# Performance work log

Measured on AMD Instinct MI355X. Metric: run time of the kernel, lower is better.

## Reference

```python
import jax, jax.numpy as jnp
import numpy as np

NCODEBOOKS, K, SUBVEC = 32, 16, 128
IN_F, OUT_F = 4096, 2048
BATCH, SEQ = 2, 1024


def setup_inputs() -> dict:
    key = jax.random.key(0)
    k1, k2, k3, k4, k5 = jax.random.split(key, 5)
    return {
        "x": jax.random.normal(k1, (BATCH, SEQ, IN_F), dtype=jnp.float32),
        "centroids": jax.random.normal(k2, (NCODEBOOKS, K, SUBVEC), dtype=jnp.float32),
        "weight": jax.random.normal(k3, (NCODEBOOKS, SUBVEC, OUT_F), dtype=jnp.float32),
        "inverse_temperature_logit": jax.random.normal(k4, (1,), dtype=jnp.float32),
        "bias": jax.random.normal(k5, (OUT_F,), dtype=jnp.float32),
    }


def reference(x, centroids, weight, inverse_temperature_logit, bias):
    shape = x.shape[:-1]
    C, k, d = centroids.shape
    # [N, C, d] -> [C, N, d]
    xr = jnp.transpose(x.reshape(-1, C, d), (1, 0, 2))
    # Euclidean cdist per codebook: [C, N, k]
    x2 = jnp.sum(xr * xr, axis=-1)[:, :, None]
    c2 = jnp.sum(centroids * centroids, axis=-1)[:, None, :]
    xc = jnp.einsum('cnd,ckd->cnk', xr, centroids)
    dist = jnp.sqrt(jnp.maximum(x2 + c2 - 2.0 * xc, 0.0))
    inv_temp = jax.nn.softplus(inverse_temperature_logit) + 1.0  # [1]
    attention = jax.nn.softmax(-dist * inv_temp, axis=-1)  # [C, N, k]
    lut = jnp.einsum('ckd,cdo->cko', centroids, weight)  # [C, k, O]
    training_output = jnp.einsum('cnk,cko->no', attention, lut)  # [N, O]
    # one-hot argmin matmul == direct gather of lut rows
    idx = jnp.argmin(dist, axis=-1)  # [C, N]
    gathered = jnp.take_along_axis(lut, idx[:, :, None], axis=1)  # [C, N, O]
    inference_output = jnp.sum(gathered, axis=0)  # [N, O]
    # straight-through estimator
    output = training_output - jax.lax.stop_gradient(training_output - inference_output)
    output = output + bias
    return output.reshape(*shape, lut.shape[-1])
```

## Files before the change

kernel.cpp:

```cpp
#include <hip/hip_runtime.h>

#define NCB 32
#define KK 16
#define DD 128
#define IN_F 4096
#define OUT_F 2048
#define NTOK 2048

#define LUT_BLOCKS 128
#define TT 32
#define IDX_BLOCKS ((NTOK / TT) * NCB)

#define XS_STRIDE 148
#define CS_OFF (TT * XS_STRIDE)
#define SMEM_FLOATS (CS_OFF + KK * 164)

__global__ __launch_bounds__(256, 4) void fused_lut_idx(
    const float* __restrict__ centroids, const float* __restrict__ weight,
    const float* __restrict__ x, const float* __restrict__ bias,
    float* __restrict__ lut, unsigned char* __restrict__ idxb) {
    __shared__ float smem[SMEM_FLOATS];
    const int tid = threadIdx.x;

    if (blockIdx.x < LUT_BLOCKS) {
        const int c  = blockIdx.x >> 2;
        const int kh = (blockIdx.x >> 1) & 1;
        const int oh = blockIdx.x & 1;
        const int o  = oh * 1024 + tid * 4;
        const float* cb = centroids + ((size_t)c * KK + kh * 8) * DD;
        const float* wb = weight + (size_t)c * DD * OUT_F + o;
        float4 acc[8];
#pragma unroll
        for (int k = 0; k < 8; ++k) acc[k] = make_float4(0.f, 0.f, 0.f, 0.f);
#pragma unroll 2
        for (int d4 = 0; d4 < DD / 4; ++d4) {
            float4 w0 = *(const float4*)(wb + (size_t)(d4 * 4 + 0) * OUT_F);
            float4 w1 = *(const float4*)(wb + (size_t)(d4 * 4 + 1) * OUT_F);
            float4 w2 = *(const float4*)(wb + (size_t)(d4 * 4 + 2) * OUT_F);
            float4 w3 = *(const float4*)(wb + (size_t)(d4 * 4 + 3) * OUT_F);
#pragma unroll
            for (int k = 0; k < 8; ++k) {
                float4 cv = *(const float4*)(cb + k * DD + d4 * 4);
                acc[k].x += cv.x * w0.x + cv.y * w1.x + cv.z * w2.x + cv.w * w3.x;
                acc[k].y += cv.x * w0.y + cv.y * w1.y + cv.z * w2.y + cv.w * w3.y;
                acc[k].z += cv.x * w0.z + cv.y * w1.z + cv.z * w2.z + cv.w * w3.z;
                acc[k].w += cv.x * w0.w + cv.y * w1.w + cv.z * w2.w + cv.w * w3.w;
            }
        }
        if (c == 0) {
            float4 bv = *(const float4*)(bias + o);
#pragma unroll
            for (int k = 0; k < 8; ++k) {
                acc[k].x += bv.x; acc[k].y += bv.y;
                acc[k].z += bv.z; acc[k].w += bv.w;
            }
        }
#pragma unroll
        for (int k = 0; k < 8; ++k)
            *(float4*)(lut + ((size_t)c * KK + kh * 8 + k) * OUT_F + o) = acc[k];
    } else {
        const int bid = blockIdx.x - LUT_BLOCKS;
        const int c = bid & (NCB - 1);
        const int t0 = (bid >> 5) * TT;
        const int th_q = tid & 3;
        const int th_k = (tid >> 2) & 3;
        const int th_t = tid >> 4;
        float* xs = smem;
        float* cs = smem + CS_OFF;

        {
            const float* xg = x + (size_t)t0 * IN_F + c * DD;
#pragma unroll
            for (int i = 0; i < (TT * DD / 4) / 256; ++i) {
                int p = i * 256 + tid;
                int t = p >> 5, f4 = p & 31;
                int q = f4 >> 3, jj = f4 & 7;
                float4 v = *(const float4*)(xg + (size_t)t * IN_F + f4 * 4);
                *(float4*)(xs + t * XS_STRIDE + q * 36 + jj * 4) = v;
            }
        }
        for (int p = tid; p < KK * 32; p += 256) {
            int k = p >> 5, f4 = p & 31;
            int q = f4 >> 3, jj = f4 & 7;
            *(float4*)(cs + k * 164 + q * 40 + jj * 4) =
                *(const float4*)(centroids + ((size_t)c * KK + k) * DD + f4 * 4);
        }
        __syncthreads();

        float acc[2][4], sq[4];
#pragma unroll
        for (int r = 0; r < 2; ++r)
#pragma unroll
            for (int kk = 0; kk < 4; ++kk) acc[r][kk] = 0.f;
#pragma unroll
        for (int kk = 0; kk < 4; ++kk) sq[kk] = 0.f;

#pragma unroll
        for (int chunk = 0; chunk < 8; ++chunk) {
            float4 ca[4];
#pragma unroll
            for (int kk = 0; kk < 4; ++kk)
                ca[kk] = *(const float4*)(cs + (th_k * 4 + kk) * 164 + th_q * 40 + chunk * 4);
#pragma unroll
            for (int kk = 0; kk < 4; ++kk)
                sq[kk] += ca[kk].x * ca[kk].x + ca[kk].y * ca[kk].y
                        + ca[kk].z * ca[kk].z + ca[kk].w * ca[kk].w;
#pragma unroll
            for (int r = 0; r < 2; ++r) {
                float4 xr = *(const float4*)(xs + (th_t * 2 + r) * XS_STRIDE
                                             + th_q * 36 + chunk * 4);
#pragma unroll
                for (int kk = 0; kk < 4; ++kk)
                    acc[r][kk] += xr.x * ca[kk].x + xr.y * ca[kk].y
                                + xr.z * ca[kk].z + xr.w * ca[kk].w;
            }
        }
#pragma unroll
        for (int kk = 0; kk < 4; ++kk) {
            float a = sq[kk];
            a += __shfl_xor(a, 1);
            a += __shfl_xor(a, 2);
            sq[kk] = a;
        }
#pragma unroll
        for (int r = 0; r < 2; ++r)
#pragma unroll
            for (int kk = 0; kk < 4; ++kk) {
                float a = acc[r][kk];
                a += __shfl_xor(a, 1);
                a += __shfl_xor(a, 2);
                acc[r][kk] = a;
            }
#pragma unroll
        for (int r = 0; r < 2; ++r) {
            float best = sq[0] - 2.f * acc[r][0];
            int bi = th_k * 4;
#pragma unroll
            for (int kk = 1; kk < 4; ++kk) {
                float v = sq[kk] - 2.f * acc[r][kk];
                if (v < best) { best = v; bi = th_k * 4 + kk; }
            }
#pragma unroll
            for (int s = 4; s <= 8; s <<= 1) {
                float ov = __shfl_xor(best, s);
                int oi = __shfl_xor(bi, s);
                if (ov < best || (ov == best && oi < bi)) { best = ov; bi = oi; }
            }
            if ((tid & 15) == 0)
                idxb[(size_t)(t0 + th_t * 2 + r) * NCB + c] = (unsigned char)bi;
        }
    }
}

__global__ __launch_bounds__(256) void gather_kernel(const float* __restrict__ lut,
                                                     const unsigned char* __restrict__ idxb,
                                                     float* __restrict__ out) {
    const int o0 = blockIdx.x * 32;
    const int t0 = blockIdx.y * 128;
    const int og = threadIdx.x & 7;
    const int tl = threadIdx.x >> 3;
    const int o = o0 + og * 4;

#pragma unroll
    for (int tt = 0; tt < 4; ++tt) {
        const int t = t0 + tt * 32 + tl;
        const uint4 iv0 = *(const uint4*)(idxb + (size_t)t * NCB);
        const uint4 iv1 = *(const uint4*)(idxb + (size_t)t * NCB + 16);
        unsigned int u[8] = {iv0.x, iv0.y, iv0.z, iv0.w, iv1.x, iv1.y, iv1.z, iv1.w};
        float4 acc = make_float4(0.f, 0.f, 0.f, 0.f);
#pragma unroll
        for (int c4 = 0; c4 < 8; ++c4) {
            unsigned int uv = u[c4];
#pragma unroll
            for (int b = 0; b < 4; ++b) {
                int cc = c4 * 4 + b;
                int k = (uv >> (8 * b)) & 0xff;
                const float4 v = *(const float4*)(lut + (size_t)(cc * KK + k) * OUT_F + o);
                acc.x += v.x; acc.y += v.y; acc.z += v.z; acc.w += v.w;
            }
        }
        *(float4*)(out + (size_t)t * OUT_F + o) = acc;
    }
}

extern "C" void kernel_launch(void* const* d_in, const int* in_sizes, int n_in,
                              void* d_out, int out_size, void* d_ws, size_t ws_size,
                              hipStream_t stream) {
    const float* x         = (const float*)d_in[0];
    const float* centroids = (const float*)d_in[1];
    const float* weight    = (const float*)d_in[2];
    const float* bias      = (const float*)d_in[4];
    float* out = (float*)d_out;

    float* lut = (float*)d_ws;
    unsigned char* idxb = (unsigned char*)d_ws + (4u << 20);

    fused_lut_idx<<<LUT_BLOCKS + IDX_BLOCKS, 256, 0, stream>>>(
        centroids, weight, x, bias, lut, idxb);
    gather_kernel<<<dim3(OUT_F / 32, NTOK / 128), 256, 0, stream>>>(lut, idxb, out);
}
```

Measured before the change: 141.0 us.

## Load x and centroids directly from global in idx path; interleave gather over two tokens

```diff
diff --git a/kernel.cpp b/kernel.cpp
--- a/kernel.cpp
+++ b/kernel.cpp
@@ -11,15 +11,10 @@
 #define TT 32
 #define IDX_BLOCKS ((NTOK / TT) * NCB)
 
-#define XS_STRIDE 148
-#define CS_OFF (TT * XS_STRIDE)
-#define SMEM_FLOATS (CS_OFF + KK * 164)
-
 __global__ __launch_bounds__(256, 4) void fused_lut_idx(
     const float* __restrict__ centroids, const float* __restrict__ weight,
     const float* __restrict__ x, const float* __restrict__ bias,
     float* __restrict__ lut, unsigned char* __restrict__ idxb) {
-    __shared__ float smem[SMEM_FLOATS];
     const int tid = threadIdx.x;
 
     if (blockIdx.x < LUT_BLOCKS) {
@@ -65,27 +60,9 @@
         const int th_q = tid & 3;
         const int th_k = (tid >> 2) & 3;
         const int th_t = tid >> 4;
-        float* xs = smem;
-        float* cs = smem + CS_OFF;
 
-        {
-            const float* xg = x + (size_t)t0 * IN_F + c * DD;
-#pragma unroll
-            for (int i = 0; i < (TT * DD / 4) / 256; ++i) {
-                int p = i * 256 + tid;
-                int t = p >> 5, f4 = p & 31;
-                int q = f4 >> 3, jj = f4 & 7;
-                float4 v = *(const float4*)(xg + (size_t)t * IN_F + f4 * 4);
-                *(float4*)(xs + t * XS_STRIDE + q * 36 + jj * 4) = v;
-            }
-        }
-        for (int p = tid; p < KK * 32; p += 256) {
-            int k = p >> 5, f4 = p & 31;
-            int q = f4 >> 3, jj = f4 & 7;
-            *(float4*)(cs + k * 164 + q * 40 + jj * 4) =
-                *(const float4*)(centroids + ((size_t)c * KK + k) * DD + f4 * 4);
-        }
-        __syncthreads();
+        const float* xg = x + (size_t)(t0 + th_t * 2) * IN_F + c * DD + th_q * 32;
+        const float* cg = centroids + ((size_t)c * KK + th_k * 4) * DD + th_q * 32;
 
         float acc[2][4], sq[4];
 #pragma unroll
@@ -100,15 +77,14 @@
             float4 ca[4];
 #pragma unroll
             for (int kk = 0; kk < 4; ++kk)
-                ca[kk] = *(const float4*)(cs + (th_k * 4 + kk) * 164 + th_q * 40 + chunk * 4);
+                ca[kk] = *(const float4*)(cg + kk * DD + chunk * 4);
 #pragma unroll
             for (int kk = 0; kk < 4; ++kk)
                 sq[kk] += ca[kk].x * ca[kk].x + ca[kk].y * ca[kk].y
                         + ca[kk].z * ca[kk].z + ca[kk].w * ca[kk].w;
 #pragma unroll
             for (int r = 0; r < 2; ++r) {
-                float4 xr = *(const float4*)(xs + (th_t * 2 + r) * XS_STRIDE
-                                             + th_q * 36 + chunk * 4);
+                float4 xr = *(const float4*)(xg + (size_t)r * IN_F + chunk * 4);
 #pragma unroll
                 for (int kk = 0; kk < 4; ++kk)
                     acc[r][kk] += xr.x * ca[kk].x + xr.y * ca[kk].y
@@ -156,31 +132,38 @@
                                                      const unsigned char* __restrict__ idxb,
                                                      float* __restrict__ out) {
     const int o0 = blockIdx.x * 32;
-    const int t0 = blockIdx.y * 128;
+    const int t0 = blockIdx.y * 64;
     const int og = threadIdx.x & 7;
     const int tl = threadIdx.x >> 3;
     const int o = o0 + og * 4;
 
+    const int ta = t0 + tl;
+    const int tb = ta + 32;
+    const uint4 ivA0 = *(const uint4*)(idxb + (size_t)ta * NCB);
+    const uint4 ivA1 = *(const uint4*)(idxb + (size_t)ta * NCB + 16);
+    const uint4 ivB0 = *(const uint4*)(idxb + (size_t)tb * NCB);
+    const uint4 ivB1 = *(const uint4*)(idxb + (size_t)tb * NCB + 16);
+    unsigned int uA[8] = {ivA0.x, ivA0.y, ivA0.z, ivA0.w, ivA1.x, ivA1.y, ivA1.z, ivA1.w};
+    unsigned int uB[8] = {ivB0.x, ivB0.y, ivB0.z, ivB0.w, ivB1.x, ivB1.y, ivB1.z, ivB1.w};
+
+    float4 accA = make_float4(0.f, 0.f, 0.f, 0.f);
+    float4 accB = make_float4(0.f, 0.f, 0.f, 0.f);
 #pragma unroll
-    for (int tt = 0; tt < 4; ++tt) {
-        const int t = t0 + tt * 32 + tl;
-        const uint4 iv0 = *(const uint4*)(idxb + (size_t)t * NCB);
-        const uint4 iv1 = *(const uint4*)(idxb + (size_t)t * NCB + 16);
-        unsigned int u[8] = {iv0.x, iv0.y, iv0.z, iv0.w, iv1.x, iv1.y, iv1.z, iv1.w};
-        float4 acc = make_float4(0.f, 0.f, 0.f, 0.f);
+    for (int c4 = 0; c4 < 8; ++c4) {
+        unsigned int uvA = uA[c4], uvB = uB[c4];
 #pragma unroll
-        for (int c4 = 0; c4 < 8; ++c4) {
-            unsigned int uv = u[c4];
-#pragma unroll
-            for (int b = 0; b < 4; ++b) {
-                int cc = c4 * 4 + b;
-                int k = (uv >> (8 * b)) & 0xff;
-                const float4 v = *(const float4*)(lut + (size_t)(cc * KK + k) * OUT_F + o);
-                acc.x += v.x; acc.y += v.y; acc.z += v.z; acc.w += v.w;
-            }
+        for (int b = 0; b < 4; ++b) {
+            int cc = c4 * 4 + b;
+            int kA = (uvA >> (8 * b)) & 0xff;
+            int kB = (uvB >> (8 * b)) & 0xff;
+            const float4 vA = *(const float4*)(lut + (size_t)(cc * KK + kA) * OUT_F + o);
+            const float4 vB = *(const float4*)(lut + (size_t)(cc * KK + kB) * OUT_F + o);
+            accA.x += vA.x; accA.y += vA.y; accA.z += vA.z; accA.w += vA.w;
+            accB.x += vB.x; accB.y += vB.y; accB.z += vB.z; accB.w += vB.w;
         }
-        *(float4*)(out + (size_t)t * OUT_F + o) = acc;
     }
+    *(float4*)(out + (size_t)ta * OUT_F + o) = accA;
+    *(float4*)(out + (size_t)tb * OUT_F + o) = accB;
 }
 
 extern "C" void kernel_launch(void* const* d_in, const int* in_sizes, int n_in,
@@ -197,5 +180,5 @@
 
     fused_lut_idx<<<LUT_BLOCKS + IDX_BLOCKS, 256, 0, stream>>>(
         centroids, weight, x, bias, lut, idxb);
-    gather_kernel<<<dim3(OUT_F / 32, NTOK / 128), 256, 0, stream>>>(lut, idxb, out);
+    gather_kernel<<<dim3(OUT_F / 32, NTOK / 64), 256, 0, stream>>>(lut, idxb, out);
 }
```

Result: slower. 172.2 us (+22.1%).
